# Kernel tuning notes

Measured on AMD Instinct MI355X. Metric: run time of the kernel, lower is better.

The kernel has to match this reference:

```python
import jax, jax.numpy as jnp
import numpy as np

H = 56; W = 56; WS = 7; SHIFT = 3; C = 256; NH = 8
HD = C // NH; N = WS * WS; NW = (H // WS) * (W // WS)
SCALE = HD ** -0.5
LN_EPS = 1e-5


def _rel_pos_index():
    coords = np.stack(np.meshgrid(np.arange(WS), np.arange(WS), indexing='ij'))  # (2, ws, ws)
    cf = coords.reshape(2, -1)
    rel = (cf[:, :, None] - cf[:, None, :]).transpose(1, 2, 0)  # (N, N, 2)
    rel[..., 0] += WS - 1
    rel[..., 1] += WS - 1
    rel[..., 0] *= 2 * WS - 1
    return rel.sum(-1)  # (N, N) indices into (2*ws-1)^2 table

RPI = jnp.asarray(_rel_pos_index())


def _attn_mask():
    img = np.zeros((H, W))
    slices = (slice(0, -WS), slice(-WS, -SHIFT), slice(-SHIFT, None))
    cnt = 0
    for hs in slices:
        for ws_ in slices:
            img[hs, ws_] = cnt
            cnt += 1
    mw = img.reshape(H // WS, WS, W // WS, WS).transpose(0, 2, 1, 3).reshape(-1, N)
    diff = mw[:, None, :] - mw[:, :, None]  # (nW, N, N), [w,i,j] = mw[w,j]-mw[w,i]
    return jnp.asarray(np.where(diff != 0, -100.0, 0.0).astype(np.float32))

AMASK = _attn_mask()  # (nW, N, N)


def ln(x, g, b):
    m = x.mean(-1, keepdims=True)
    v = x.var(-1, keepdims=True)
    return (x - m) / jnp.sqrt(v + LN_EPS) * g + b


def win_part(x):  # (B, H, W, C) -> (B*nW, N, C)
    B = x.shape[0]
    return x.reshape(B, H // WS, WS, W // WS, WS, C).transpose(0, 1, 3, 2, 4, 5).reshape(-1, N, C)


def win_rev(xw, B):  # (B*nW, N, C) -> (B, H, W, C)
    return xw.reshape(B, H // WS, W // WS, WS, WS, C).transpose(0, 1, 3, 2, 4, 5).reshape(B, H, W, C)


def setup_inputs() -> dict:
    key = jax.random.key(0)
    ks = iter(jax.random.split(key, 40))
    B, L = 16, H * W
    Ch = int(C * 4.0)
    p = {}
    p['x'] = jax.random.normal(next(ks), (B, L, C), jnp.float32)
    p['x_SAR'] = jax.random.normal(next(ks), (B, L, C), jnp.float32)
    p['ln1_g'] = jnp.ones((C,)); p['ln1_b'] = jnp.zeros((C,))
    p['ln1s_g'] = jnp.ones((C,)); p['ln1s_b'] = jnp.zeros((C,))
    p['qkv_w'] = jax.random.normal(next(ks), (3 * C, C)) * 0.02
    p['qkv_b'] = jnp.zeros((3 * C,))
    p['qkvs_w'] = jax.random.normal(next(ks), (3 * C, C)) * 0.02
    p['qkvs_b'] = jnp.zeros((3 * C,))
    p['rpb_table'] = jax.random.normal(next(ks), ((2 * WS - 1) ** 2, NH)) * 0.02
    p['fuse_w'] = jax.random.normal(next(ks), (NH, NH)) * 0.1  # Conv2d(8,8,1) weight squeezed
    p['fuse_b'] = jnp.zeros((NH,))
    p['proj_w'] = jax.random.normal(next(ks), (C, C)) * 0.02
    p['proj_b'] = jnp.zeros((C,))
    p['projs_w'] = jax.random.normal(next(ks), (C, C)) * 0.02
    p['projs_b'] = jnp.zeros((C,))
    p['ln2_g'] = jnp.ones((C,)); p['ln2_b'] = jnp.zeros((C,))
    p['ln2s_g'] = jnp.ones((C,)); p['ln2s_b'] = jnp.zeros((C,))
    p['fc1_w'] = jax.random.normal(next(ks), (Ch, C)) * 0.02
    p['fc1_b'] = jnp.zeros((Ch,))
    p['fc2_w'] = jax.random.normal(next(ks), (C, Ch)) * 0.02
    p['fc2_b'] = jnp.zeros((C,))
    p['fc1s_w'] = jax.random.normal(next(ks), (Ch, C)) * 0.02
    p['fc1s_b'] = jnp.zeros((Ch,))
    p['fc2s_w'] = jax.random.normal(next(ks), (C, Ch)) * 0.02
    p['fc2s_b'] = jnp.zeros((C,))
    return p


def reference(x, x_SAR, ln1_g, ln1_b, ln1s_g, ln1s_b, qkv_w, qkv_b, qkvs_w, qkvs_b,
              rpb_table, fuse_w, fuse_b, proj_w, proj_b, projs_w, projs_b,
              ln2_g, ln2_b, ln2s_g, ln2s_b, fc1_w, fc1_b, fc2_w, fc2_b,
              fc1s_w, fc1s_b, fc2s_w, fc2s_b):
    B = x.shape[0]
    sc, sc_s = x, x_SAR

    def pre(xx, g, b):  # norm -> spatial -> cyclic shift -> windows
        xs = ln(xx, g, b).reshape(B, H, W, C)
        xs = jnp.roll(xs, (-SHIFT, -SHIFT), axis=(1, 2))
        return win_part(xs)

    xw = pre(x, ln1_g, ln1_b)
    xws = pre(x_SAR, ln1s_g, ln1s_b)

    def qkv_f(xin, Wt, bt):
        qkv = (xin @ Wt.T + bt).reshape(-1, N, 3, NH, HD).transpose(2, 0, 3, 1, 4)
        return qkv[0], qkv[1], qkv[2]  # each (B*nW, nH, N, HD)

    q, k, v = qkv_f(xw, qkv_w, qkv_b)
    qs, ks_, vs = qkv_f(xws, qkvs_w, qkvs_b)

    attn = jnp.einsum('bhnd,bhmd->bhnm', q * SCALE, k)
    attn_s = jnp.einsum('bhnd,bhmd->bhnm', qs * SCALE, ks_)

    rpb = rpb_table[RPI.reshape(-1)].reshape(N, N, NH).transpose(2, 0, 1)  # (nH, N, N)
    attn = attn + rpb[None]
    attn_s = attn_s + rpb[None]

    # shift-window mask add
    attn = (attn.reshape(B, NW, NH, N, N) + AMASK[None, :, None]).reshape(-1, NH, N, N)
    attn_s = (attn_s.reshape(B, NW, NH, N, N) + AMASK[None, :, None]).reshape(-1, NH, N, N)

    # dual-branch fusion: 1x1 conv over head dim + sigmoid gate
    diff = attn_s - attn
    gate = jax.nn.sigmoid(jnp.einsum('oh,bhnm->bonm', fuse_w, diff) + fuse_b[None, :, None, None])
    attn_f = jax.nn.softmax(attn + diff * gate, axis=-1)
    attn_s = jax.nn.softmax(attn_s, axis=-1)

    def out_f(a, vv, pw, pb):
        o = jnp.einsum('bhnm,bhmd->bhnd', a, vv).transpose(0, 2, 1, 3).reshape(-1, N, C)
        return o @ pw.T + pb

    xo = out_f(attn_f, v, proj_w, proj_b)
    xos = out_f(attn_s, vs, projs_w, projs_b)

    def post(xout, scc, g2, b2, w1, b1, w2, b2m):
        xr = jnp.roll(win_rev(xout, B), (SHIFT, SHIFT), axis=(1, 2)).reshape(B, -1, C)
        xr = scc + xr
        h = jax.nn.gelu(ln(xr, g2, b2) @ w1.T + b1, approximate=False)
        return xr + (h @ w2.T + b2m)

    out = post(xo, sc, ln2_g, ln2_b, fc1_w, fc1_b, fc2_w, fc2_b)
    out_s = post(xos, sc_s, ln2s_g, ln2s_b, fc1s_w, fc1s_b, fc2s_w, fc2s_b)
    return out, out_s
```

## Files before the change

kernel.cpp:

```cpp
#include <hip/hip_runtime.h>
#include <hip/hip_bf16.h>
#include <cstdio>

typedef unsigned short ushort_t;
using bf16x8  = __attribute__((ext_vector_type(8))) __bf16;
using floatx4 = __attribute__((ext_vector_type(4))) float;

constexpr int    kTokens = 50176;
constexpr size_t TCsz    = (size_t)kTokens * 256;
constexpr float  kScale  = 0.17677669529663687f;
constexpr int    SPITCH  = 56;
constexpr size_t SPAIR   = 49 * 56;
constexpr size_t SBUFSZ  = (size_t)8192 * SPAIR;

__device__ __forceinline__ float bf2f(ushort_t u) {
  unsigned int x = (unsigned int)u << 16;
  return __uint_as_float(x);
}
__device__ __forceinline__ ushort_t f2bf(float f) {
  __hip_bfloat16 h = __float2bfloat16(f);
  return *(ushort_t*)&h;
}

__device__ __forceinline__ void gl_lds16(const ushort_t* g, ushort_t* l) {
  __builtin_amdgcn_global_load_lds(
      (const __attribute__((address_space(1))) unsigned int*)g,
      (__attribute__((address_space(3))) unsigned int*)l, 16, 0, 0);
}

__global__ __launch_bounds__(256) void f2b_k(const float* __restrict__ src,
                                             ushort_t* __restrict__ dst, int n) {
  int i = blockIdx.x * 256 + threadIdx.x;
  if (i < n) dst[i] = f2bf(src[i]);
}

__global__ __launch_bounds__(256) void bias_k(const float* __restrict__ rpb,
                                              float* __restrict__ bias,
                                              ushort_t* __restrict__ guard) {
  const int cls = blockIdx.x >> 3, head = blockIdx.x & 7;
  const int wh7 = cls >> 1, ww7 = cls & 1;
  float* bp = bias + (size_t)blockIdx.x * SPAIR;
  for (int e = threadIdx.x; e < (int)SPAIR; e += 256) {
    const int i = e / SPITCH, j = e % SPITCH;
    float val = 0.0f;
    if (j < 49) {
      const int yi = i / 7, xi = i % 7, yj = j / 7, xj = j % 7;
      val = rpb[((yi - yj + 6) * 13 + (xi - xj + 6)) * 8 + head];
      const int li = (wh7 ? (yi < 4 ? 1 : 2) : 0) * 3 + (ww7 ? (xi < 4 ? 1 : 2) : 0);
      const int lj = (wh7 ? (yj < 4 ? 1 : 2) : 0) * 3 + (ww7 ? (xj < 4 ? 1 : 2) : 0);
      if (li != lj) val -= 100.0f;
    }
    bp[e] = val;
  }
  if (blockIdx.x == 0 && threadIdx.x < 64) guard[threadIdx.x] = 0;
}

template <int SHIFTED>
__global__ __launch_bounds__(256) void ln_k(const float* __restrict__ x,
                                            const float* __restrict__ g,
                                            const float* __restrict__ b,
                                            ushort_t* __restrict__ yout) {
  const int wave = threadIdx.x >> 6, lane = threadIdx.x & 63;
  const int t = blockIdx.x * 4 + wave;
  size_t src;
  if (SHIFTED) {
    int bb = t / 3136, r = t % 3136;
    int wi = r / 49, n = r % 49;
    int hp = (wi >> 3) * 7 + n / 7;
    int wp = (wi & 7) * 7 + n % 7;
    int sh = hp + 3; if (sh >= 56) sh -= 56;
    int sw = wp + 3; if (sw >= 56) sw -= 56;
    src = ((size_t)bb * 3136 + sh * 56 + sw) * 256;
  } else {
    src = (size_t)t * 256;
  }
  const float4 v4 = *(const float4*)(x + src + lane * 4);
  float s  = v4.x + v4.y + v4.z + v4.w;
  float s2 = v4.x * v4.x + v4.y * v4.y + v4.z * v4.z + v4.w * v4.w;
#pragma unroll
  for (int off = 32; off > 0; off >>= 1) {
    s  += __shfl_xor(s,  off);
    s2 += __shfl_xor(s2, off);
  }
  const float mean = s * (1.0f / 256.0f);
  const float var  = s2 * (1.0f / 256.0f) - mean * mean;
  const float rstd = rsqrtf(var + 1e-5f);
  const float4 g4 = *(const float4*)(g + lane * 4);
  const float4 b4 = *(const float4*)(b + lane * 4);
  ushort4 o;
  o.x = f2bf((v4.x - mean) * rstd * g4.x + b4.x);
  o.y = f2bf((v4.y - mean) * rstd * g4.y + b4.y);
  o.z = f2bf((v4.z - mean) * rstd * g4.z + b4.z);
  o.w = f2bf((v4.w - mean) * rstd * g4.w + b4.w);
  *(ushort4*)(yout + (size_t)t * 256 + lane * 4) = o;
}

template <int MODE>
__global__ __launch_bounds__(256) void bgemm_k(const ushort_t* __restrict__ A,
                                               const ushort_t* __restrict__ W,
                                               const float* __restrict__ bias,
                                               float* __restrict__ outf,
                                               ushort_t* __restrict__ outb,
                                               const float* __restrict__ aux,
                                               int K, int Nc) {
  __shared__ __align__(16) ushort_t As[128 * 32];
  __shared__ __align__(16) ushort_t Bs[128 * 32];
  const int tid = threadIdx.x;
  const int nbx = gridDim.x;
  const int nwg = nbx * gridDim.y;
  int flat = blockIdx.y * nbx + blockIdx.x;
  {
    const int xcd = flat & 7, idx = flat >> 3;
    const int q8 = nwg >> 3, r8 = nwg & 7;
    flat = (xcd < r8 ? xcd * (q8 + 1) : r8 * (q8 + 1) + (xcd - r8) * q8) + idx;
  }
  const int m0 = (flat / nbx) * 128;
  const int n0 = (flat % nbx) * 128;
  const int lane = tid & 63, wv = tid >> 6;
  const int wm = (wv >> 1) * 64, wn = (wv & 1) * 64;
  const int l16 = lane & 15, quad = lane >> 4;

  const int srow = tid >> 2;
  const int gkc  = (tid & 3) ^ ((tid >> 3) & 3);
  const ushort_t* Ag0 = A + (size_t)(m0 + srow) * K + gkc * 8;
  const ushort_t* Ag1 = A + (size_t)(m0 + 64 + srow) * K + gkc * 8;
  const ushort_t* Wg0 = W + (size_t)(n0 + srow) * K + gkc * 8;
  const ushort_t* Wg1 = W + (size_t)(n0 + 64 + srow) * K + gkc * 8;
  ushort_t* AsW0 = As + wv * 512;
  ushort_t* AsW1 = As + 2048 + wv * 512;
  ushort_t* BsW0 = Bs + wv * 512;
  ushort_t* BsW1 = Bs + 2048 + wv * 512;

  const int kcq = quad ^ ((l16 >> 1) & 3);
  const int arA = (wm + l16) * 32 + kcq * 8;
  const int arB = (wn + l16) * 32 + kcq * 8;

  floatx4 acc[4][4] = {};
  for (int k0 = 0; k0 < K; k0 += 32) {
    gl_lds16(Ag0, AsW0);
    gl_lds16(Ag1, AsW1);
    gl_lds16(Wg0, BsW0);
    gl_lds16(Wg1, BsW1);
    Ag0 += 32; Ag1 += 32; Wg0 += 32; Wg1 += 32;
    __syncthreads();
    bf16x8 af[4], bfr[4];
#pragma unroll
    for (int t = 0; t < 4; ++t) {
      af[t]  = *(const bf16x8*)&As[arA + t * 512];
      bfr[t] = *(const bf16x8*)&Bs[arB + t * 512];
    }
#pragma unroll
    for (int mt = 0; mt < 4; ++mt)
#pragma unroll
      for (int nt = 0; nt < 4; ++nt)
        acc[mt][nt] = __builtin_amdgcn_mfma_f32_16x16x32_bf16(af[mt], bfr[nt], acc[mt][nt], 0, 0, 0);
    __syncthreads();
  }

  if (MODE == 0) {
    size_t rb[16];
#pragma unroll
    for (int mt = 0; mt < 4; ++mt) {
      int row = m0 + wm + mt * 16 + quad * 4;
      int wi = row / 49, n = row - wi * 49;
#pragma unroll
      for (int r = 0; r < 4; ++r) {
        rb[mt * 4 + r] = (size_t)wi * 12544 + (size_t)n * 32;
        if (++n == 49) { n = 0; ++wi; }
      }
    }
#pragma unroll
    for (int nt = 0; nt < 4; ++nt) {
      const int col = n0 + wn + nt * 16 + l16;
      const int which = col >> 8, head = (col >> 5) & 7, d = col & 31;
      const float bv = bias[col];
      const float sc = (which == 0) ? kScale : 1.0f;
      ushort_t* ob = outb + (size_t)which * TCsz + head * 1568 + d;
#pragma unroll
      for (int i = 0; i < 16; ++i)
        ob[rb[i]] = f2bf((acc[i >> 2][nt][i & 3] + bv) * sc);
    }
  } else if (MODE == 1) {
    size_t rb[16];
#pragma unroll
    for (int mt = 0; mt < 4; ++mt) {
#pragma unroll
      for (int r = 0; r < 4; ++r) {
        const int row = m0 + wm + mt * 16 + quad * 4 + r;
        const int wi = row / 49, n = row - wi * 49;
        const int b = wi >> 6, wl = wi & 63;
        int h = (wl >> 3) * 7 + n / 7 + 3; if (h >= 56) h -= 56;
        int w = (wl & 7) * 7 + n % 7 + 3; if (w >= 56) w -= 56;
        rb[mt * 4 + r] = ((size_t)(b * 3136 + h * 56 + w)) * 256;
      }
    }
#pragma unroll
    for (int nt = 0; nt < 4; ++nt) {
      const int col = n0 + wn + nt * 16 + l16;
      const float bv = bias[col];
#pragma unroll
      for (int i = 0; i < 16; ++i) {
        const size_t idx = rb[i] + col;
        outf[idx] = aux[idx] + acc[i >> 2][nt][i & 3] + bv;
      }
    }
  } else if (MODE == 2) {
    size_t rb[16];
#pragma unroll
    for (int mt = 0; mt < 4; ++mt)
#pragma unroll
      for (int r = 0; r < 4; ++r)
        rb[mt * 4 + r] = (size_t)(m0 + wm + mt * 16 + quad * 4 + r) * Nc;
#pragma unroll
    for (int nt = 0; nt < 4; ++nt) {
      const int col = n0 + wn + nt * 16 + l16;
      const float bv = bias[col];
#pragma unroll
      for (int i = 0; i < 16; ++i) {
        float val = acc[i >> 2][nt][i & 3] + bv;
        val = 0.5f * val * (1.0f + erff(val * 0.70710678118654752f));
        outb[rb[i] + col] = f2bf(val);
      }
    }
  } else {
    size_t rb[16];
#pragma unroll
    for (int mt = 0; mt < 4; ++mt)
#pragma unroll
      for (int r = 0; r < 4; ++r)
        rb[mt * 4 + r] = (size_t)(m0 + wm + mt * 16 + quad * 4 + r) * 256;
#pragma unroll
    for (int nt = 0; nt < 4; ++nt) {
      const int col = n0 + wn + nt * 16 + l16;
      const float bv = bias[col];
#pragma unroll
      for (int i = 0; i < 16; ++i) {
        const size_t idx = rb[i] + col;
        outf[idx] = aux[idx] + acc[i >> 2][nt][i & 3] + bv;
      }
    }
  }
}

__global__ __launch_bounds__(256) void scores_mfma_k(const ushort_t* __restrict__ q,
                                                     const ushort_t* __restrict__ k,
                                                     const float* __restrict__ bias,
                                                     ushort_t* __restrict__ S) {
  const int tid = threadIdx.x, lane = tid & 63, wv = tid >> 6;
  const int pair = blockIdx.x * 4 + wv;
  const int head = pair & 7, win = pair >> 3;
  const int l16 = lane & 15, quad = lane >> 4;
  const ushort_t* qb = q + (size_t)pair * 1568;
  const ushort_t* kb = k + (size_t)pair * 1568;
  bf16x8 af[4], bfr[4];
#pragma unroll
  for (int t = 0; t < 4; ++t) {
    af[t]  = *(const bf16x8*)(qb + (t * 16 + l16) * 32 + quad * 8);
    bfr[t] = *(const bf16x8*)(kb + (t * 16 + l16) * 32 + quad * 8);
  }
  floatx4 acc[4][4] = {};
#pragma unroll
  for (int mt = 0; mt < 4; ++mt)
#pragma unroll
    for (int nt = 0; nt < 4; ++nt)
      acc[mt][nt] = __builtin_amdgcn_mfma_f32_16x16x32_bf16(af[mt], bfr[nt], acc[mt][nt], 0, 0, 0);

  const int wl = win & 63;
  const int cls = (((wl >> 3) == 7) ? 2 : 0) + (((wl & 7) == 7) ? 1 : 0);
  const float* bp = bias + (size_t)(cls * 8 + head) * SPAIR;
  ushort_t* Sp = S + (size_t)pair * SPAIR;
#pragma unroll
  for (int nt = 0; nt < 4; ++nt) {
    const int col = nt * 16 + l16;
    if (col >= SPITCH) continue;
#pragma unroll
    for (int mt = 0; mt < 4; ++mt) {
#pragma unroll
      for (int r = 0; r < 4; ++r) {
        const int row = mt * 16 + quad * 4 + r;
        if (row >= 49) continue;
        const float val = (col < 49) ? acc[mt][nt][r] + bp[row * SPITCH + col] : 0.0f;
        Sp[row * SPITCH + col] = f2bf(val);
      }
    }
  }
}

__global__ __launch_bounds__(256) void fuse2_k(ushort_t* __restrict__ S,
                                               ushort_t* __restrict__ Ss,
                                               const float* __restrict__ fw,
                                               const float* __restrict__ fb) {
  __shared__ float s[8][637], ss[8][637];
  __shared__ float fwl[64], fbl[8];
  const int w = blockIdx.x >> 2, ch = blockIdx.x & 3;
  const int n0 = ch * 13;
  const int rows = (n0 + 13 <= 49) ? 13 : (49 - n0);
  const int cnt = 8 * rows * 49;
  const int tid = threadIdx.x;
  if (tid < 64) fwl[tid] = fw[tid];
  if (tid < 8)  fbl[tid] = fb[tid];
  for (int t = tid; t < cnt; t += 256) {
    const int h = t / (rows * 49), rm = t % (rows * 49);
    const int r = rm / 49, c = rm - r * 49;
    const size_t gaddr = (size_t)(w * 8 + h) * SPAIR + (size_t)(n0 + r) * SPITCH + c;
    s[h][rm]  = bf2f(S[gaddr]);
    ss[h][rm] = bf2f(Ss[gaddr]);
  }
  __syncthreads();
  for (int p = tid; p < rows * 49; p += 256) {
    float d[8];
#pragma unroll
    for (int h = 0; h < 8; ++h) d[h] = ss[h][p] - s[h][p];
#pragma unroll
    for (int o = 0; o < 8; ++o) {
      float g = fbl[o];
#pragma unroll
      for (int h = 0; h < 8; ++h) g = fmaf(fwl[o * 8 + h], d[h], g);
      g = 1.0f / (1.0f + expf(-g));
      s[o][p] = s[o][p] + d[o] * g;
    }
  }
  __syncthreads();
  if (tid < 16 * rows) {
    const int br = tid / (8 * rows);
    const int hr = tid % (8 * rows);
    const int h = hr / rows, r = hr % rows;
    float* row = (br ? ss[h] : s[h]) + r * 49;
    float mx = -1e30f;
    for (int m = 0; m < 49; ++m) mx = fmaxf(mx, row[m]);
    float sum = 0.0f;
    for (int m = 0; m < 49; ++m) { float e = expf(row[m] - mx); row[m] = e; sum += e; }
    const float inv = 1.0f / sum;
    for (int m = 0; m < 49; ++m) row[m] *= inv;
  }
  __syncthreads();
  for (int t = tid; t < cnt; t += 256) {
    const int h = t / (rows * 49), rm = t % (rows * 49);
    const int r = rm / 49, c = rm - r * 49;
    const size_t gaddr = (size_t)(w * 8 + h) * SPAIR + (size_t)(n0 + r) * SPITCH + c;
    S[gaddr]  = f2bf(s[h][rm]);
    Ss[gaddr] = f2bf(ss[h][rm]);
  }
}

__global__ __launch_bounds__(256) void pv_mfma_k(const ushort_t* __restrict__ P,
                                                 const ushort_t* __restrict__ v,
                                                 ushort_t* __restrict__ O) {
  __shared__ __align__(16) ushort_t vt[4][32][72];
  const int tid = threadIdx.x, lane = tid & 63, wv = tid >> 6;
  const int pair = blockIdx.x * 4 + wv;
  const int head = pair & 7, win = pair >> 3;
  const int l16 = lane & 15, quad = lane >> 4;
  const ushort_t* vb = v + (size_t)pair * 1568;
  for (int e = lane; e < 736; e += 64) {
    const int d = e / 23, m = 49 + e % 23;
    vt[wv][d][m] = 0;
  }
  for (int e = lane; e < 1568; e += 64) {
    vt[wv][e & 31][e >> 5] = vb[e];
  }
  __syncthreads();
  bf16x8 bfr[2][2];
#pragma unroll
  for (int nt = 0; nt < 2; ++nt)
#pragma unroll
    for (int ks = 0; ks < 2; ++ks)
      bfr[nt][ks] = *(const bf16x8*)&vt[wv][nt * 16 + l16][ks * 32 + quad * 8];

  const ushort_t* Pb = P + (size_t)pair * SPAIR;
  floatx4 acc[4][2] = {};
#pragma unroll
  for (int ks = 0; ks < 2; ++ks) {
#pragma unroll
    for (int mt = 0; mt < 4; ++mt) {
      const bf16x8 af = *(const bf16x8*)(Pb + (size_t)(mt * 16 + l16) * SPITCH + ks * 32 + quad * 8);
#pragma unroll
      for (int nt = 0; nt < 2; ++nt)
        acc[mt][nt] = __builtin_amdgcn_mfma_f32_16x16x32_bf16(af, bfr[nt][ks], acc[mt][nt], 0, 0, 0);
    }
  }
#pragma unroll
  for (int mt = 0; mt < 4; ++mt) {
#pragma unroll
    for (int r = 0; r < 4; ++r) {
      const int n = mt * 16 + quad * 4 + r;
      if (n >= 49) continue;
      const size_t base = ((size_t)(win * 49 + n)) * 256 + head * 32;
#pragma unroll
      for (int nt = 0; nt < 2; ++nt)
        O[base + nt * 16 + l16] = f2bf(acc[mt][nt][r]);
    }
  }
}

extern "C" void kernel_launch(void* const* d_in, const int* in_sizes, int n_in,
                              void* d_out, int out_size, void* d_ws, size_t ws_size,
                              hipStream_t stream) {
  if (n_in < 29) { fprintf(stderr, "kernel_launch: expected 29 inputs, got %d\n", n_in); return; }
  const float* x      = (const float*)d_in[0];
  const float* xsar   = (const float*)d_in[1];
  const float* ln1_g  = (const float*)d_in[2];
  const float* ln1_b  = (const float*)d_in[3];
  const float* ln1s_g = (const float*)d_in[4];
  const float* ln1s_b = (const float*)d_in[5];
  const float* qkv_w  = (const float*)d_in[6];
  const float* qkv_b  = (const float*)d_in[7];
  const float* qkvs_w = (const float*)d_in[8];
  const float* qkvs_b = (const float*)d_in[9];
  const float* rpb    = (const float*)d_in[10];
  const float* fuse_w = (const float*)d_in[11];
  const float* fuse_b = (const float*)d_in[12];
  const float* proj_w = (const float*)d_in[13];
  const float* proj_b = (const float*)d_in[14];
  const float* projs_w = (const float*)d_in[15];
  const float* projs_b = (const float*)d_in[16];
  const float* ln2_g  = (const float*)d_in[17];
  const float* ln2_b  = (const float*)d_in[18];
  const float* ln2s_g = (const float*)d_in[19];
  const float* ln2s_b = (const float*)d_in[20];
  const float* fc1_w  = (const float*)d_in[21];
  const float* fc1_b  = (const float*)d_in[22];
  const float* fc2_w  = (const float*)d_in[23];
  const float* fc2_b  = (const float*)d_in[24];
  const float* fc1s_w = (const float*)d_in[25];
  const float* fc1s_b = (const float*)d_in[26];
  const float* fc2s_w = (const float*)d_in[27];
  const float* fc2s_b = (const float*)d_in[28];
  float* out = (float*)d_out;
  float* ws  = (float*)d_ws;

  const size_t need = 8 * TCsz * sizeof(float);
  if (ws_size < need) {
    fprintf(stderr, "kernel_launch: ws_size %zu < needed %zu\n", ws_size, need);
    return;
  }

  ushort_t* H   = (ushort_t*)ws;
  ushort_t* xw  = H;
  ushort_t* xws = H + TCsz;
  ushort_t* q   = H + 2 * TCsz;
  ushort_t* qs  = H + 5 * TCsz;
  ushort_t* v_  = H + 4 * TCsz;
  ushort_t* vs  = H + 7 * TCsz;
  ushort_t* SA  = H + 8 * TCsz;
  ushort_t* SB  = SA + SBUFSZ;
  ushort_t* guard = SB + SBUFSZ;
  float* xr  = ws + 6 * TCsz;
  float* xrs = ws + 7 * TCsz;
  ushort_t* y   = H + 2 * TCsz;
  ushort_t* ysb = H + 3 * TCsz;
  ushort_t* hbuf = H + 4 * TCsz;
  ushort_t* wb  = H + 12 * TCsz - 1572864;
  float* biasbuf = (float*)(H + 12 * TCsz - 1572864 - 175616);
  ushort_t* wqkv  = wb;
  ushort_t* wqkvs = wb + 196608;
  ushort_t* wproj = wb + 393216;
  ushort_t* wprojs= wb + 458752;
  ushort_t* wfc1  = wb + 524288;
  ushort_t* wfc1s = wb + 786432;
  ushort_t* wfc2  = wb + 1048576;
  ushort_t* wfc2s = wb + 1310720;

  f2b_k<<<768, 256, 0, stream>>>(qkv_w,  wqkv,  196608);
  f2b_k<<<768, 256, 0, stream>>>(qkvs_w, wqkvs, 196608);
  f2b_k<<<256, 256, 0, stream>>>(proj_w, wproj, 65536);
  f2b_k<<<256, 256, 0, stream>>>(projs_w,wprojs,65536);
  f2b_k<<<1024,256, 0, stream>>>(fc1_w,  wfc1,  262144);
  f2b_k<<<1024,256, 0, stream>>>(fc1s_w, wfc1s, 262144);
  f2b_k<<<1024,256, 0, stream>>>(fc2_w,  wfc2,  262144);
  f2b_k<<<1024,256, 0, stream>>>(fc2s_w, wfc2s, 262144);
  bias_k<<<32, 256, 0, stream>>>(rpb, biasbuf, guard);

  ln_k<1><<<12544, 256, 0, stream>>>(x,    ln1_g,  ln1_b,  xw);
  ln_k<1><<<12544, 256, 0, stream>>>(xsar, ln1s_g, ln1s_b, xws);
  bgemm_k<0><<<dim3(6, 392), 256, 0, stream>>>(xw,  wqkv,  qkv_b,  nullptr, q,  nullptr, 256, 768);
  bgemm_k<0><<<dim3(6, 392), 256, 0, stream>>>(xws, wqkvs, qkvs_b, nullptr, qs, nullptr, 256, 768);
  scores_mfma_k<<<2048, 256, 0, stream>>>(q,  q + TCsz,  biasbuf, SA);
  scores_mfma_k<<<2048, 256, 0, stream>>>(qs, qs + TCsz, biasbuf, SB);
  fuse2_k<<<4096, 256, 0, stream>>>(SA, SB, fuse_w, fuse_b);
  pv_mfma_k<<<2048, 256, 0, stream>>>(SA, v_, H);
  pv_mfma_k<<<2048, 256, 0, stream>>>(SB, vs, H + TCsz);
  bgemm_k<1><<<dim3(2, 392), 256, 0, stream>>>(H,          wproj,  proj_b,  xr,  nullptr, x,    256, 256);
  bgemm_k<1><<<dim3(2, 392), 256, 0, stream>>>(H + TCsz,   wprojs, projs_b, xrs, nullptr, xsar, 256, 256);
  ln_k<0><<<12544, 256, 0, stream>>>(xr,  ln2_g,  ln2_b,  y);
  ln_k<0><<<12544, 256, 0, stream>>>(xrs, ln2s_g, ln2s_b, ysb);
  bgemm_k<2><<<dim3(8, 392), 256, 0, stream>>>(y,    wfc1,  fc1_b,  nullptr, hbuf, nullptr, 256, 1024);
  bgemm_k<3><<<dim3(2, 392), 256, 0, stream>>>(hbuf, wfc2,  fc2_b,  out,     nullptr, xr,  1024, 256);
  bgemm_k<2><<<dim3(8, 392), 256, 0, stream>>>(ysb,  wfc1s, fc1s_b, nullptr, hbuf, nullptr, 256, 1024);
  bgemm_k<3><<<dim3(2, 392), 256, 0, stream>>>(hbuf, wfc2s, fc2s_b, out + TCsz, nullptr, xrs, 1024, 256);
}
```

Before: 969.9 us.

## Fuse scores, gated dual-branch fusion, softmax and PV into one LDS-resident attention kernel

Replaces the separate scores, fuse, and PV kernels with a single attention kernel. Each block handles a 16-row chunk of one window for all 8 heads of both branches and keeps the score tiles in shared memory, so the large bf16 score buffers are never written to or read back from global memory. The QKV GEMM epilogue now writes V pre-transposed into a padded per-head layout, and a small kernel zeroes that padding, which removes the per-block LDS transpose in PV. The trade-offs are bf16 rounding of the fused scores inside LDS, redundant K and V loads across the four row chunks, and fast exp and reciprocal intrinsics in place of the exact ones.

```diff
diff --git a/kernel.cpp b/kernel.cpp
--- a/kernel.cpp
+++ b/kernel.cpp
@@ -11,7 +11,8 @@
 constexpr float  kScale  = 0.17677669529663687f;
 constexpr int    SPITCH  = 56;
 constexpr size_t SPAIR   = 49 * 56;
-constexpr size_t SBUFSZ  = (size_t)8192 * SPAIR;
+constexpr size_t VTP     = 2048;
+constexpr size_t VTSZ    = (size_t)8192 * VTP;
 
 __device__ __forceinline__ float bf2f(ushort_t u) {
   unsigned int x = (unsigned int)u << 16;
@@ -35,8 +36,7 @@
 }
 
 __global__ __launch_bounds__(256) void bias_k(const float* __restrict__ rpb,
-                                              float* __restrict__ bias,
-                                              ushort_t* __restrict__ guard) {
+                                              float* __restrict__ bias) {
   const int cls = blockIdx.x >> 3, head = blockIdx.x & 7;
   const int wh7 = cls >> 1, ww7 = cls & 1;
   float* bp = bias + (size_t)blockIdx.x * SPAIR;
@@ -52,7 +52,16 @@
     }
     bp[e] = val;
   }
-  if (blockIdx.x == 0 && threadIdx.x < 64) guard[threadIdx.x] = 0;
+}
+
+__global__ __launch_bounds__(256) void vtz_k(ushort_t* __restrict__ vtA,
+                                             ushort_t* __restrict__ vtB) {
+  const int id = blockIdx.x * 256 + threadIdx.x;
+  ushort_t* base = (id < 262144) ? vtA : vtB;
+  const size_t r = (size_t)(id & 262143) * 64;
+  const uint4 z{0, 0, 0, 0};
+  *(uint4*)(base + r + 48) = z;
+  *(uint4*)(base + r + 56) = z;
 }
 
 template <int SHIFTED>
@@ -158,27 +167,47 @@
   }
 
   if (MODE == 0) {
-    size_t rb[16];
+    int wis[16], ns[16];
 #pragma unroll
     for (int mt = 0; mt < 4; ++mt) {
       int row = m0 + wm + mt * 16 + quad * 4;
       int wi = row / 49, n = row - wi * 49;
 #pragma unroll
       for (int r = 0; r < 4; ++r) {
-        rb[mt * 4 + r] = (size_t)wi * 12544 + (size_t)n * 32;
+        wis[mt * 4 + r] = wi; ns[mt * 4 + r] = n;
         if (++n == 49) { n = 0; ++wi; }
       }
     }
-#pragma unroll
-    for (int nt = 0; nt < 4; ++nt) {
-      const int col = n0 + wn + nt * 16 + l16;
-      const int which = col >> 8, head = (col >> 5) & 7, d = col & 31;
-      const float bv = bias[col];
-      const float sc = (which == 0) ? kScale : 1.0f;
-      ushort_t* ob = outb + (size_t)which * TCsz + head * 1568 + d;
-#pragma unroll
-      for (int i = 0; i < 16; ++i)
-        ob[rb[i]] = f2bf((acc[i >> 2][nt][i & 3] + bv) * sc);
+    if (n0 < 512) {
+      size_t rb[16];
+#pragma unroll
+      for (int i = 0; i < 16; ++i) rb[i] = (size_t)wis[i] * 12544 + (size_t)ns[i] * 32;
+#pragma unroll
+      for (int nt = 0; nt < 4; ++nt) {
+        const int col = n0 + wn + nt * 16 + l16;
+        const int which = col >> 8, head = (col >> 5) & 7, d = col & 31;
+        const float bv = bias[col];
+        const float sc = (which == 0) ? kScale : 1.0f;
+        ushort_t* ob = outb + (size_t)which * TCsz + head * 1568 + d;
+#pragma unroll
+        for (int i = 0; i < 16; ++i)
+          ob[rb[i]] = f2bf((acc[i >> 2][nt][i & 3] + bv) * sc);
+      }
+    } else {
+      size_t rb[16];
+#pragma unroll
+      for (int i = 0; i < 16; ++i) rb[i] = (size_t)wis[i] * 16384 + (size_t)ns[i];
+      ushort_t* vtb = (ushort_t*)outf;
+#pragma unroll
+      for (int nt = 0; nt < 4; ++nt) {
+        const int col = n0 + wn + nt * 16 + l16;
+        const int head = (col >> 5) & 7, d = col & 31;
+        const float bv = bias[col];
+        ushort_t* ob = vtb + head * 2048 + d * 64;
+#pragma unroll
+        for (int i = 0; i < 16; ++i)
+          ob[rb[i]] = f2bf(acc[i >> 2][nt][i & 3] + bv);
+      }
     }
   } else if (MODE == 1) {
     size_t rb[16];
@@ -242,154 +271,123 @@
   }
 }
 
-__global__ __launch_bounds__(256) void scores_mfma_k(const ushort_t* __restrict__ q,
-                                                     const ushort_t* __restrict__ k,
-                                                     const float* __restrict__ bias,
-                                                     ushort_t* __restrict__ S) {
+__global__ __launch_bounds__(256) void attn_k(const ushort_t* __restrict__ qA,
+                                              const ushort_t* __restrict__ qB,
+                                              const ushort_t* __restrict__ vtA,
+                                              const ushort_t* __restrict__ vtB,
+                                              const float* __restrict__ bias,
+                                              const float* __restrict__ fw,
+                                              const float* __restrict__ fb,
+                                              ushort_t* __restrict__ Obase) {
+  __shared__ __align__(16) ushort_t S[16 * 16 * 56 + 64];
+  __shared__ float fwl[64], fbl[8];
   const int tid = threadIdx.x, lane = tid & 63, wv = tid >> 6;
-  const int pair = blockIdx.x * 4 + wv;
-  const int head = pair & 7, win = pair >> 3;
   const int l16 = lane & 15, quad = lane >> 4;
-  const ushort_t* qb = q + (size_t)pair * 1568;
-  const ushort_t* kb = k + (size_t)pair * 1568;
-  bf16x8 af[4], bfr[4];
-#pragma unroll
-  for (int t = 0; t < 4; ++t) {
-    af[t]  = *(const bf16x8*)(qb + (t * 16 + l16) * 32 + quad * 8);
-    bfr[t] = *(const bf16x8*)(kb + (t * 16 + l16) * 32 + quad * 8);
-  }
-  floatx4 acc[4][4] = {};
-#pragma unroll
-  for (int mt = 0; mt < 4; ++mt)
-#pragma unroll
-    for (int nt = 0; nt < 4; ++nt)
-      acc[mt][nt] = __builtin_amdgcn_mfma_f32_16x16x32_bf16(af[mt], bfr[nt], acc[mt][nt], 0, 0, 0);
+  int bx = blockIdx.x;
+  bx = (bx & 7) * 512 + (bx >> 3);
+  const int win = bx >> 2, chunk = bx & 3;
+  const int r0 = chunk * 16;
+  const int rows = (r0 + 16 <= 49) ? 16 : (49 - r0);
+  {
+    uint4* p4 = (uint4*)S;
+    for (int i = tid; i < 1800; i += 256) p4[i] = uint4{0, 0, 0, 0};
+  }
+  if (tid < 64) fwl[tid] = fw[tid];
+  if (tid < 8)  fbl[tid] = fb[tid];
+  __syncthreads();
 
   const int wl = win & 63;
   const int cls = (((wl >> 3) == 7) ? 2 : 0) + (((wl & 7) == 7) ? 1 : 0);
-  const float* bp = bias + (size_t)(cls * 8 + head) * SPAIR;
-  ushort_t* Sp = S + (size_t)pair * SPAIR;
-#pragma unroll
-  for (int nt = 0; nt < 4; ++nt) {
-    const int col = nt * 16 + l16;
-    if (col >= SPITCH) continue;
-#pragma unroll
-    for (int mt = 0; mt < 4; ++mt) {
+
+  const int qrow = (r0 + l16 <= 48) ? (r0 + l16) : 48;
+  for (int i = 0; i < 4; ++i) {
+    const int pair = wv * 4 + i;
+    const int br = pair >> 3, h = pair & 7;
+    const ushort_t* qb = (br ? qB : qA) + (size_t)(win * 8 + h) * 1568;
+    const ushort_t* kb = qb + TCsz;
+    const bf16x8 af = *(const bf16x8*)(qb + qrow * 32 + quad * 8);
+    floatx4 acc[4];
+#pragma unroll
+    for (int nt = 0; nt < 4; ++nt) {
+      const int krow = nt * 16 + l16;
+      const int krc = (krow <= 48) ? krow : 48;
+      const bf16x8 bfr = *(const bf16x8*)(kb + krc * 32 + quad * 8);
+      acc[nt] = __builtin_amdgcn_mfma_f32_16x16x32_bf16(af, bfr, (floatx4){0.f, 0.f, 0.f, 0.f}, 0, 0, 0);
+    }
+    const float* bp = bias + (size_t)(cls * 8 + h) * SPAIR;
+    ushort_t* Sp = S + pair * 896;
+#pragma unroll
+    for (int nt = 0; nt < 4; ++nt) {
+      const int col = nt * 16 + l16;
+      if (col >= SPITCH) continue;
 #pragma unroll
       for (int r = 0; r < 4; ++r) {
-        const int row = mt * 16 + quad * 4 + r;
-        if (row >= 49) continue;
-        const float val = (col < 49) ? acc[mt][nt][r] + bp[row * SPITCH + col] : 0.0f;
-        Sp[row * SPITCH + col] = f2bf(val);
-      }
-    }
-  }
-}
-
-__global__ __launch_bounds__(256) void fuse2_k(ushort_t* __restrict__ S,
-                                               ushort_t* __restrict__ Ss,
-                                               const float* __restrict__ fw,
-                                               const float* __restrict__ fb) {
-  __shared__ float s[8][637], ss[8][637];
-  __shared__ float fwl[64], fbl[8];
-  const int w = blockIdx.x >> 2, ch = blockIdx.x & 3;
-  const int n0 = ch * 13;
-  const int rows = (n0 + 13 <= 49) ? 13 : (49 - n0);
-  const int cnt = 8 * rows * 49;
-  const int tid = threadIdx.x;
-  if (tid < 64) fwl[tid] = fw[tid];
-  if (tid < 8)  fbl[tid] = fb[tid];
-  for (int t = tid; t < cnt; t += 256) {
-    const int h = t / (rows * 49), rm = t % (rows * 49);
-    const int r = rm / 49, c = rm - r * 49;
-    const size_t gaddr = (size_t)(w * 8 + h) * SPAIR + (size_t)(n0 + r) * SPITCH + c;
-    s[h][rm]  = bf2f(S[gaddr]);
-    ss[h][rm] = bf2f(Ss[gaddr]);
+        const int lrow = quad * 4 + r;
+        if (lrow < rows)
+          Sp[lrow * 56 + col] = (col < 49) ? f2bf(acc[nt][r] + bp[(r0 + lrow) * 56 + col]) : (ushort_t)0;
+      }
+    }
   }
   __syncthreads();
-  for (int p = tid; p < rows * 49; p += 256) {
-    float d[8];
-#pragma unroll
-    for (int h = 0; h < 8; ++h) d[h] = ss[h][p] - s[h][p];
+
+  const int np = rows * 49;
+  for (int p = tid; p < np; p += 256) {
+    const int lr = p / 49, c = p - lr * 49;
+    const int off = lr * 56 + c;
+    float sA[8], dd[8];
+#pragma unroll
+    for (int h = 0; h < 8; ++h) {
+      sA[h] = bf2f(S[h * 896 + off]);
+      dd[h] = bf2f(S[(8 + h) * 896 + off]) - sA[h];
+    }
 #pragma unroll
     for (int o = 0; o < 8; ++o) {
       float g = fbl[o];
 #pragma unroll
-      for (int h = 0; h < 8; ++h) g = fmaf(fwl[o * 8 + h], d[h], g);
-      g = 1.0f / (1.0f + expf(-g));
-      s[o][p] = s[o][p] + d[o] * g;
+      for (int h = 0; h < 8; ++h) g = fmaf(fwl[o * 8 + h], dd[h], g);
+      g = __builtin_amdgcn_rcpf(1.0f + __expf(-g));
+      S[o * 896 + off] = f2bf(sA[o] + dd[o] * g);
     }
   }
   __syncthreads();
-  if (tid < 16 * rows) {
-    const int br = tid / (8 * rows);
-    const int hr = tid % (8 * rows);
-    const int h = hr / rows, r = hr % rows;
-    float* row = (br ? ss[h] : s[h]) + r * 49;
-    float mx = -1e30f;
-    for (int m = 0; m < 49; ++m) mx = fmaxf(mx, row[m]);
-    float sum = 0.0f;
-    for (int m = 0; m < 49; ++m) { float e = expf(row[m] - mx); row[m] = e; sum += e; }
-    const float inv = 1.0f / sum;
-    for (int m = 0; m < 49; ++m) row[m] *= inv;
+
+  {
+    const int lr = tid & 15, ph = tid >> 4;
+    if (lr < rows) {
+      ushort_t* row = S + ph * 896 + lr * 56;
+      float mx = -1e30f;
+      for (int m = 0; m < 49; ++m) mx = fmaxf(mx, bf2f(row[m]));
+      float sum = 0.0f;
+      for (int m = 0; m < 49; ++m) sum += __expf(bf2f(row[m]) - mx);
+      const float inv = __builtin_amdgcn_rcpf(sum);
+      for (int m = 0; m < 49; ++m) row[m] = f2bf(__expf(bf2f(row[m]) - mx) * inv);
+    }
   }
   __syncthreads();
-  for (int t = tid; t < cnt; t += 256) {
-    const int h = t / (rows * 49), rm = t % (rows * 49);
-    const int r = rm / 49, c = rm - r * 49;
-    const size_t gaddr = (size_t)(w * 8 + h) * SPAIR + (size_t)(n0 + r) * SPITCH + c;
-    S[gaddr]  = f2bf(s[h][rm]);
-    Ss[gaddr] = f2bf(ss[h][rm]);
-  }
-}
-
-__global__ __launch_bounds__(256) void pv_mfma_k(const ushort_t* __restrict__ P,
-                                                 const ushort_t* __restrict__ v,
-                                                 ushort_t* __restrict__ O) {
-  __shared__ __align__(16) ushort_t vt[4][32][72];
-  const int tid = threadIdx.x, lane = tid & 63, wv = tid >> 6;
-  const int pair = blockIdx.x * 4 + wv;
-  const int head = pair & 7, win = pair >> 3;
-  const int l16 = lane & 15, quad = lane >> 4;
-  const ushort_t* vb = v + (size_t)pair * 1568;
-  for (int e = lane; e < 736; e += 64) {
-    const int d = e / 23, m = 49 + e % 23;
-    vt[wv][d][m] = 0;
-  }
-  for (int e = lane; e < 1568; e += 64) {
-    vt[wv][e & 31][e >> 5] = vb[e];
-  }
-  __syncthreads();
-  bf16x8 bfr[2][2];
-#pragma unroll
-  for (int nt = 0; nt < 2; ++nt)
-#pragma unroll
-    for (int ks = 0; ks < 2; ++ks)
-      bfr[nt][ks] = *(const bf16x8*)&vt[wv][nt * 16 + l16][ks * 32 + quad * 8];
-
-  const ushort_t* Pb = P + (size_t)pair * SPAIR;
-  floatx4 acc[4][2] = {};
-#pragma unroll
-  for (int ks = 0; ks < 2; ++ks) {
-#pragma unroll
-    for (int mt = 0; mt < 4; ++mt) {
-      const bf16x8 af = *(const bf16x8*)(Pb + (size_t)(mt * 16 + l16) * SPITCH + ks * 32 + quad * 8);
-#pragma unroll
-      for (int nt = 0; nt < 2; ++nt)
-        acc[mt][nt] = __builtin_amdgcn_mfma_f32_16x16x32_bf16(af, bfr[nt][ks], acc[mt][nt], 0, 0, 0);
-    }
-  }
-#pragma unroll
-  for (int mt = 0; mt < 4; ++mt) {
-#pragma unroll
-    for (int r = 0; r < 4; ++r) {
-      const int n = mt * 16 + quad * 4 + r;
-      if (n >= 49) continue;
-      const size_t base = ((size_t)(win * 49 + n)) * 256 + head * 32;
-#pragma unroll
-      for (int nt = 0; nt < 2; ++nt)
-        O[base + nt * 16 + l16] = f2bf(acc[mt][nt][r]);
-    }
+
+  for (int i = 0; i < 4; ++i) {
+    const int pair = wv * 4 + i;
+    const int br = pair >> 3, h = pair & 7;
+    const ushort_t* vt = (br ? vtB : vtA) + (size_t)(win * 8 + h) * VTP;
+    const ushort_t* Sp = S + pair * 896;
+    floatx4 acc[2] = {};
+#pragma unroll
+    for (int ks = 0; ks < 2; ++ks) {
+      const bf16x8 af = *(const bf16x8*)(Sp + l16 * 56 + ks * 32 + quad * 8);
+#pragma unroll
+      for (int nt = 0; nt < 2; ++nt) {
+        const bf16x8 bv = *(const bf16x8*)(vt + (nt * 16 + l16) * 64 + ks * 32 + quad * 8);
+        acc[nt] = __builtin_amdgcn_mfma_f32_16x16x32_bf16(af, bv, acc[nt], 0, 0, 0);
+      }
+    }
+    ushort_t* Ob = Obase + (size_t)br * TCsz + (size_t)(win * 49 + r0) * 256 + h * 32;
+#pragma unroll
+    for (int nt = 0; nt < 2; ++nt)
+#pragma unroll
+      for (int r = 0; r < 4; ++r) {
+        const int n = quad * 4 + r;
+        if (n < rows) Ob[(size_t)n * 256 + nt * 16 + l16] = f2bf(acc[nt][r]);
+      }
   }
 }
 
@@ -440,11 +438,8 @@
   ushort_t* xws = H + TCsz;
   ushort_t* q   = H + 2 * TCsz;
   ushort_t* qs  = H + 5 * TCsz;
-  ushort_t* v_  = H + 4 * TCsz;
-  ushort_t* vs  = H + 7 * TCsz;
-  ushort_t* SA  = H + 8 * TCsz;
-  ushort_t* SB  = SA + SBUFSZ;
-  ushort_t* guard = SB + SBUFSZ;
+  ushort_t* vtA = H + 8 * TCsz;
+  ushort_t* vtB = vtA + VTSZ;
   float* xr  = ws + 6 * TCsz;
   float* xrs = ws + 7 * TCsz;
   ushort_t* y   = H + 2 * TCsz;
@@ -469,19 +464,16 @@
   f2b_k<<<1024,256, 0, stream>>>(fc1s_w, wfc1s, 262144);
   f2b_k<<<1024,256, 0, stream>>>(fc2_w,  wfc2,  262144);
   f2b_k<<<1024,256, 0, stream>>>(fc2s_w, wfc2s, 262144);
-  bias_k<<<32, 256, 0, stream>>>(rpb, biasbuf, guard);
+  bias_k<<<32, 256, 0, stream>>>(rpb, biasbuf);
+  vtz_k<<<2048, 256, 0, stream>>>(vtA, vtB);
 
   ln_k<1><<<12544, 256, 0, stream>>>(x,    ln1_g,  ln1_b,  xw);
   ln_k<1><<<12544, 256, 0, stream>>>(xsar, ln1s_g, ln1s_b, xws);
-  bgemm_k<0><<<dim3(6, 392), 256, 0, stream>>>(xw,  wqkv,  qkv_b,  nullptr, q,  nullptr, 256, 768);
-  bgemm_k<0><<<dim3(6, 392), 256, 0, stream>>>(xws, wqkvs, qkvs_b, nullptr, qs, nullptr, 256, 768);
-  scores_mfma_k<<<2048, 256, 0, stream>>>(q,  q + TCsz,  biasbuf, SA);
-  scores_mfma_k<<<2048, 256, 0, stream>>>(qs, qs + TCsz, biasbuf, SB);
-  fuse2_k<<<4096, 256, 0, stream>>>(SA, SB, fuse_w, fuse_b);
-  pv_mfma_k<<<2048, 256, 0, stream>>>(SA, v_, H);
-  pv_mfma_k<<<2048, 256, 0, stream>>>(SB, vs, H + TCsz);
-  bgemm_k<1><<<dim3(2, 392), 256, 0, stream>>>(H,          wproj,  proj_b,  xr,  nullptr, x,    256, 256);
-  bgemm_k<1><<<dim3(2, 392), 256, 0, stream>>>(H + TCsz,   wprojs, projs_b, xrs, nullptr, xsar, 256, 256);
+  bgemm_k<0><<<dim3(6, 392), 256, 0, stream>>>(xw,  wqkv,  qkv_b,  (float*)vtA, q,  nullptr, 256, 768);
+  bgemm_k<0><<<dim3(6, 392), 256, 0, stream>>>(xws, wqkvs, qkvs_b, (float*)vtB, qs, nullptr, 256, 768);
+  attn_k<<<4096, 256, 0, stream>>>(q, qs, vtA, vtB, biasbuf, fuse_w, fuse_b, H);
+  bgemm_k<1><<<dim3(2, 392), 256, 0, stream>>>(H,        wproj,  proj_b,  xr,  nullptr, x,    256, 256);
+  bgemm_k<1><<<dim3(2, 392), 256, 0, stream>>>(H + TCsz, wprojs, projs_b, xrs, nullptr, xsar, 256, 256);
   ln_k<0><<<12544, 256, 0, stream>>>(xr,  ln2_g,  ln2_b,  y);
   ln_k<0><<<12544, 256, 0, stream>>>(xrs, ln2s_g, ln2s_b, ysb);
   bgemm_k<2><<<dim3(8, 392), 256, 0, stream>>>(y,    wfc1,  fc1_b,  nullptr, hbuf, nullptr, 256, 1024);
```

Result: no change. 970.4 us (+0.0%).
